# Optimization experiments

Measured on AMD Instinct MI355X. Metric: run time of the kernel, lower is better.

## Reference

```python
import jax, jax.numpy as jnp
import numpy as np

B, C, H, W = 16, 768, 32, 32
NH, HD, STRIDE = 12, 64, 2
ORF = 2.0  # offset_range_factor
EPS = 1e-5


def dwconv(x, w, b, s):
    # depthwise 3x3 conv, NCHW, weight [C,1,3,3]
    y = jax.lax.conv_general_dilated(
        x, w, window_strides=(s, s), padding=((1, 1), (1, 1)),
        dimension_numbers=('NCHW', 'OIHW', 'NCHW'), feature_group_count=x.shape[1])
    return y + b[None, :, None, None]


def layernorm_c(x, g, b):
    # LayerNorm over channel dim of NCHW (via bhwc as in LayerNormProxy)
    xt = jnp.transpose(x, (0, 2, 3, 1))
    mu = jnp.mean(xt, axis=-1, keepdims=True)
    var = jnp.mean((xt - mu) ** 2, axis=-1, keepdims=True)
    xn = (xt - mu) / jnp.sqrt(var + EPS)
    return jnp.transpose(xn * g + b, (0, 3, 1, 2))


def ref_points(Hh, Ww):
    # matches torch linspace(0.5, H-0.5, H)/H*2-1, stacked as (y, x)
    ry = (jnp.arange(Hh, dtype=jnp.float32) + 0.5) / Hh * 2.0 - 1.0
    rx = (jnp.arange(Ww, dtype=jnp.float32) + 0.5) / Ww * 2.0 - 1.0
    yy, xx = jnp.meshgrid(ry, rx, indexing='ij')
    return jnp.stack([yy, xx], axis=-1)  # [H, W, 2]


def grid_sample_bilinear(inp, grid):
    # inp [B,Cc,Hi,Wi], grid [B,Hg,Wg,2] in (x,y), align_corners=True, zeros padding
    Bb, Cc, Hi, Wi = inp.shape
    gx = (grid[..., 0] + 1.0) * (Wi - 1) * 0.5
    gy = (grid[..., 1] + 1.0) * (Hi - 1) * 0.5
    x0 = jnp.floor(gx); y0 = jnp.floor(gy)
    wx = gx - x0; wy = gy - y0

    def gather(iy, ix):
        valid = (ix >= 0) & (ix <= Wi - 1) & (iy >= 0) & (iy <= Hi - 1)
        iyc = jnp.clip(iy, 0, Hi - 1).astype(jnp.int32)
        ixc = jnp.clip(ix, 0, Wi - 1).astype(jnp.int32)
        vals = jax.vmap(lambda img, a, b: img[:, a, b])(inp, iyc, ixc)  # [B,Cc,Hg,Wg]
        return vals * valid[:, None, :, :].astype(inp.dtype)

    w00 = ((1 - wy) * (1 - wx))[:, None]
    w01 = ((1 - wy) * wx)[:, None]
    w10 = (wy * (1 - wx))[:, None]
    w11 = (wy * wx)[:, None]
    return (gather(y0, x0) * w00 + gather(y0, x0 + 1) * w01
            + gather(y0 + 1, x0) * w10 + gather(y0 + 1, x0 + 1) * w11)


def setup_inputs() -> dict:
    key = jax.random.key(0)
    ks = jax.random.split(key, 16)
    n = lambda k, shp, s: jax.random.normal(k, shp, jnp.float32) * s
    Hk = H // STRIDE
    return {
        'x': n(ks[0], (B, C, H, W), 1.0),
        'wv': n(ks[1], (C, 1, 3, 3), 0.1), 'bv': jnp.zeros((C,), jnp.float32),
        'wq': n(ks[2], (C, 1, 3, 3), 0.1), 'bq': jnp.zeros((C,), jnp.float32),
        'wk': n(ks[3], (C, 1, 3, 3), 0.1), 'bk': jnp.zeros((C,), jnp.float32),
        'w_off1': n(ks[4], (C, 1, 3, 3), 0.1), 'b_off1': jnp.zeros((C,), jnp.float32),
        'ln_g': jnp.ones((C,), jnp.float32), 'ln_b': jnp.zeros((C,), jnp.float32),
        'w_off2': n(ks[5], (2, C, 1, 1), 0.02),
        'rpe_table': n(ks[6], (NH, 2 * Hk - 1, 2 * Hk - 1), 0.01),
        'w_out': n(ks[7], (C, C, 1, 1), 0.02),
    }


def reference(x, wv, bv, wq, bq, wk, bk, w_off1, b_off1, ln_g, ln_b, w_off2, rpe_table, w_out):
    scale = HD ** -0.5
    value = dwconv(x, wv, bv, 1)          # [B,C,H,W]
    query = dwconv(x, wq, bq, 1)          # [B,C,H,W]
    keym = dwconv(x, wk, bk, STRIDE)      # [B,C,Hk,Wk]
    # offset branch: dwconv -> LN -> GELU -> 1x1 conv to 2 channels
    t = jax.nn.gelu(layernorm_c(dwconv(x, w_off1, b_off1, STRIDE), ln_g, ln_b), approximate=False)
    off = jnp.einsum('bchw,pc->bphw', t, w_off2.reshape(2, C))  # [B,2,Hk,Wk] (y,x)
    Hk, Wk = off.shape[2], off.shape[3]
    ns = Hk * Wk
    orange = jnp.array([1.0 / Hk, 1.0 / Wk], jnp.float32).reshape(1, 2, 1, 1)
    off = jnp.tanh(off) * orange * ORF
    off = jnp.transpose(off, (0, 2, 3, 1))  # [B,Hk,Wk,2]
    pos = off + ref_points(Hk, Wk)[None]    # [B,Hk,Wk,2] (y,x); ORF>0 -> no extra tanh

    vs = grid_sample_bilinear(value, pos[..., ::-1]).reshape(B * NH, HD, ns)
    q = query.reshape(B * NH, HD, H * W)
    k = keym.reshape(B * NH, HD, ns)
    attn = jnp.einsum('bcm,bcn->bmn', q, k) * scale  # [B*NH, HW, ns]

    # continuous relative position bias via grid_sample on rpe table
    rpe_bias = jnp.broadcast_to(rpe_table[None], (B, NH, 2 * Hk - 1, 2 * Wk - 1))
    qg = ref_points(H, W).reshape(H * W, 2)
    disp = (qg[None, :, None, :] - pos.reshape(B, ns, 2)[:, None, :, :]) * 0.5  # [B,HW,ns,2]
    bias = grid_sample_bilinear(rpe_bias, disp[..., ::-1]).reshape(B * NH, H * W, ns)

    attn = jax.nn.softmax(attn + bias, axis=-1)
    out = jnp.einsum('bmn,bcn->bcm', attn, vs).reshape(B, C, H, W)
    return jnp.einsum('bchw,oc->bohw', out, w_out.reshape(C, C))
```

## Files before the change

kernel.cpp:

```cpp
#include <hip/hip_runtime.h>
#include <hip/hip_bf16.h>
#include <math.h>

typedef unsigned short u16;
typedef __attribute__((ext_vector_type(8))) short bf8_t;
typedef __attribute__((ext_vector_type(4))) float f4_t;

#define BB 16
#define CC 768
#define HH 32
#define WW 32
#define HWL 1024
#define NHH 12
#define HDD 64
#define HK 16
#define NS 256
#define RT 31

__device__ inline float us2f(u16 u) {
    return __uint_as_float(((unsigned int)u) << 16);
}
__device__ inline u16 f2us(float f) {
    unsigned int u = __float_as_uint(f);
    unsigned int r = (u + 0x7fffu + ((u >> 16) & 1u)) >> 16;
    return (u16)r;
}

__global__ __launch_bounds__(256) void k_dwconv(
    const float* __restrict__ x,
    const float* __restrict__ wv, const float* __restrict__ bv,
    const float* __restrict__ wq, const float* __restrict__ bq,
    const float* __restrict__ wk, const float* __restrict__ bk,
    const float* __restrict__ wo, const float* __restrict__ bo,
    u16* __restrict__ value, u16* __restrict__ query,
    u16* __restrict__ key, float* __restrict__ tbuf)
{
    __shared__ float xs[34 * 34];
    int blk = blockIdx.x;
    int b = blk / CC, c = blk % CC;
    int tid = threadIdx.x;
    const float* xp = x + (size_t)(b * CC + c) * HWL;

    for (int i = tid; i < 34 * 34; i += 256) {
        int r = i / 34, cc2 = i % 34;
        int gr = r - 1, gc = cc2 - 1;
        float v = 0.f;
        if (gr >= 0 && gr < 32 && gc >= 0 && gc < 32) v = xp[gr * 32 + gc];
        xs[i] = v;
    }
    float wv_[9], wq_[9], wk_[9], wo_[9];
#pragma unroll
    for (int k = 0; k < 9; ++k) {
        wv_[k] = wv[c * 9 + k];
        wq_[k] = wq[c * 9 + k];
        wk_[k] = wk[c * 9 + k];
        wo_[k] = wo[c * 9 + k];
    }
    float bv_ = bv[c], bq_ = bq[c], bk_ = bk[c], bo_ = bo[c];
    __syncthreads();

    {
        int oy = tid >> 3;
        int ox4 = (tid & 7) * 4;
        float xw[3][6];
#pragma unroll
        for (int dy = 0; dy < 3; ++dy)
#pragma unroll
            for (int dx = 0; dx < 6; ++dx)
                xw[dy][dx] = xs[(oy + dy) * 34 + ox4 + dx];
        union { u16 u[4]; ushort4 v; } pv, pq;
#pragma unroll
        for (int j = 0; j < 4; ++j) {
            float av = 0.f, aq = 0.f;
#pragma unroll
            for (int dy = 0; dy < 3; ++dy)
#pragma unroll
                for (int dx = 0; dx < 3; ++dx) {
                    float xv = xw[dy][j + dx];
                    av += xv * wv_[dy * 3 + dx];
                    aq += xv * wq_[dy * 3 + dx];
                }
            pv.u[j] = f2us(av + bv_);
            pq.u[j] = f2us(aq + bq_);
        }
        size_t o = (size_t)(b * CC + c) * HWL + oy * 32 + ox4;
        *(ushort4*)&value[o] = pv.v;
        *(ushort4*)&query[o] = pq.v;
    }
    {
        int oy = tid >> 4, ox = tid & 15;
        float ak = 0.f, ao2 = 0.f;
#pragma unroll
        for (int dy = 0; dy < 3; ++dy)
#pragma unroll
            for (int dx = 0; dx < 3; ++dx) {
                float xv = xs[(2 * oy + dy) * 34 + 2 * ox + dx];
                ak += xv * wk_[dy * 3 + dx];
                ao2 += xv * wo_[dy * 3 + dx];
            }
        key[(size_t)(b * CC + c) * NS + tid] = f2us(ak + bk_);
        tbuf[(size_t)(b * CC + c) * NS + tid] = ao2 + bo_;
    }
}

__global__ __launch_bounds__(256) void k_offset(
    const float* __restrict__ tbuf,
    const float* __restrict__ lng, const float* __restrict__ lnb,
    const float* __restrict__ woff2, float* __restrict__ pos)
{
    __shared__ float sm[16];
    int blk = blockIdx.x;
    int b = blk >> 8;
    int n = blk & 255;
    int tid = threadIdx.x;
    const float* tp = tbuf + (size_t)b * CC * NS + n;
    float tv0 = tp[(size_t)tid * NS];
    float tv1 = tp[(size_t)(tid + 256) * NS];
    float tv2 = tp[(size_t)(tid + 512) * NS];
    float s = tv0 + tv1 + tv2;
    float sq = tv0 * tv0 + tv1 * tv1 + tv2 * tv2;
    for (int o = 32; o; o >>= 1) { s += __shfl_down(s, o); sq += __shfl_down(sq, o); }
    int w = tid >> 6;
    if ((tid & 63) == 0) { sm[w] = s; sm[4 + w] = sq; }
    __syncthreads();
    float st = sm[0] + sm[1] + sm[2] + sm[3];
    float sqt = sm[4] + sm[5] + sm[6] + sm[7];
    float mean = st * (1.f / 768.f);
    float var = sqt * (1.f / 768.f) - mean * mean;
    float rstd = rsqrtf(fmaxf(var, 0.f) + 1e-5f);

    float oy = 0.f, ox = 0.f;
#pragma unroll
    for (int j = 0; j < 3; ++j) {
        int c = tid + j * 256;
        float tvj = (j == 0) ? tv0 : ((j == 1) ? tv1 : tv2);
        float xn = (tvj - mean) * rstd;
        float y = xn * lng[c] + lnb[c];
        float ge = 0.5f * y * (1.f + erff(y * 0.70710678118654752f));
        oy += ge * woff2[c];
        ox += ge * woff2[CC + c];
    }
    for (int o = 32; o; o >>= 1) { oy += __shfl_down(oy, o); ox += __shfl_down(ox, o); }
    __syncthreads();
    if ((tid & 63) == 0) { sm[w] = oy; sm[8 + w] = ox; }
    __syncthreads();
    if (tid == 0) {
        float oyt = sm[0] + sm[1] + sm[2] + sm[3];
        float oxt = sm[8] + sm[9] + sm[10] + sm[11];
        float offy = tanhf(oyt) * 0.125f;
        float offx = tanhf(oxt) * 0.125f;
        int ky = n >> 4, kx = n & 15;
        pos[blk * 2 + 0] = (ky + 0.5f) * 0.125f - 1.f + offy;
        pos[blk * 2 + 1] = (kx + 0.5f) * 0.125f - 1.f + offx;
    }
}

__global__ __launch_bounds__(256) void k_sample(
    const u16* __restrict__ value, const float* __restrict__ pos,
    u16* __restrict__ vst)
{
    __shared__ float psl[NS * 2];
    int cg = blockIdx.x;
    int b  = blockIdx.y;
    int tid = threadIdx.x;
    for (int i = tid; i < NS * 2; i += 256) psl[i] = pos[b * NS * 2 + i];
    __syncthreads();
    int c = cg * 4 + (tid >> 6);
    int nl = tid & 63;
    const u16* vp = value + (size_t)(b * CC + c) * HWL;
    u16* op = vst + (size_t)(b * CC + c) * NS;
#pragma unroll
    for (int j = 0; j < 4; ++j) {
        int n = j * 64 + nl;
        float py = psl[2 * n], px = psl[2 * n + 1];
        float gx = (px + 1.f) * 15.5f;
        float gy = (py + 1.f) * 15.5f;
        float fx = floorf(gx), fy = floorf(gy);
        float wx = gx - fx, wy = gy - fy;
        int ix0 = (int)fx, iy0 = (int)fy;
        int ix1 = ix0 + 1, iy1 = iy0 + 1;
        float m00 = ((unsigned)ix0 < 32u && (unsigned)iy0 < 32u) ? 1.f : 0.f;
        float m01 = ((unsigned)ix1 < 32u && (unsigned)iy0 < 32u) ? 1.f : 0.f;
        float m10 = ((unsigned)ix0 < 32u && (unsigned)iy1 < 32u) ? 1.f : 0.f;
        float m11 = ((unsigned)ix1 < 32u && (unsigned)iy1 < 32u) ? 1.f : 0.f;
        int cx0 = min(max(ix0, 0), 31), cx1 = min(max(ix1, 0), 31);
        int cy0 = min(max(iy0, 0), 31), cy1 = min(max(iy1, 0), 31);
        float w00 = (1.f - wy) * (1.f - wx) * m00;
        float w01 = (1.f - wy) * wx * m01;
        float w10 = wy * (1.f - wx) * m10;
        float w11 = wy * wx * m11;
        float r = w00 * us2f(vp[cy0 * 32 + cx0]) + w01 * us2f(vp[cy0 * 32 + cx1])
                + w10 * us2f(vp[cy1 * 32 + cx0]) + w11 * us2f(vp[cy1 * 32 + cx1]);
        op[n] = f2us(r);
    }
}

__global__ __launch_bounds__(256) void k_transpose(
    const u16* __restrict__ in, u16* __restrict__ out, int R, int S)
{
    __shared__ u16 tile[64][68];
    int bx = blockIdx.x;
    int by = blockIdx.y;
    int bz = blockIdx.z;
    int t = threadIdx.x;
    int ci = (t & 15) * 4;
    int ri = t >> 4;
    const u16* ip = in + (size_t)bz * R * S;
    u16* op = out + (size_t)bz * R * S;
#pragma unroll
    for (int i = 0; i < 4; ++i) {
        int r = ri + i * 16;
        ushort4 v = *(const ushort4*)(ip + (size_t)(by * 64 + r) * S + bx * 64 + ci);
        *(ushort4*)&tile[r][ci] = v;
    }
    __syncthreads();
#pragma unroll
    for (int i = 0; i < 4; ++i) {
        int s = ri + i * 16;
        ushort4 v;
        v.x = tile[ci + 0][s];
        v.y = tile[ci + 1][s];
        v.z = tile[ci + 2][s];
        v.w = tile[ci + 3][s];
        *(ushort4*)(op + (size_t)(bx * 64 + s) * R + by * 64 + ci) = v;
    }
}

__global__ __launch_bounds__(256) void k_cvtw(
    const float* __restrict__ w, u16* __restrict__ wbf)
{
    int i = (blockIdx.x * 256 + threadIdx.x) * 4;
    float4 v = *(const float4*)(w + i);
    union { u16 u[4]; ushort4 v; } pk;
    pk.u[0] = f2us(v.x); pk.u[1] = f2us(v.y);
    pk.u[2] = f2us(v.z); pk.u[3] = f2us(v.w);
    *(ushort4*)(wbf + i) = pk.v;
}

__global__ __launch_bounds__(256, 4) void k_attn(
    const u16* __restrict__ query, const u16* __restrict__ kt,
    const u16* __restrict__ vst, const float* __restrict__ rpe,
    const float* __restrict__ pos, u16* __restrict__ ao)
{
    __shared__ float2 tabp2[35 * 36];
    __shared__ float2 psl2[NS];
    __shared__ u16 Plds[4][16][72];

    int L = blockIdx.x;
    int xcd = L & 7;
    int t2 = L >> 3;
    int mt = t2 & 15;
    int bh = xcd + 8 * (t2 >> 4);
    int b = bh / NHH, h = bh % NHH;
    int tid = threadIdx.x;
    int w = tid >> 6;
    int l = tid & 63;
    int li = l & 15, lg4 = l >> 4;

    for (int i = tid; i < 35 * 36; i += 256) {
        int r = i / 36, c = i % 36;
        int rr = r - 2;
        int c0i = c - 2, c1i = c - 1;
        float v0 = ((unsigned)rr < 31u && (unsigned)c0i < 31u)
                       ? rpe[h * RT * RT + rr * RT + c0i] : 0.f;
        float v1 = ((unsigned)rr < 31u && (unsigned)c1i < 31u)
                       ? rpe[h * RT * RT + rr * RT + c1i] : 0.f;
        tabp2[i] = make_float2(v0, v1);
    }
    for (int i = tid; i < NS; i += 256) {
        psl2[i] = make_float2(pos[b * NS * 2 + 2 * i], pos[b * NS * 2 + 2 * i + 1]);
    }
    __syncthreads();

    int m0 = mt * 64 + w * 16;
    int c0 = h * 64;

    bf8_t qf[2];
#pragma unroll
    for (int ks = 0; ks < 2; ++ks) {
        union { short s[8]; bf8_t v; } u;
#pragma unroll
        for (int j = 0; j < 8; ++j)
            u.s[j] = (short)query[(size_t)(b * CC + c0 + ks * 32 + lg4 * 8 + j) * HWL + m0 + li];
        qf[ks] = u.v;
    }
    bf8_t ones;
    {
        union { short s[8]; bf8_t v; } u;
#pragma unroll
        for (int j = 0; j < 8; ++j) u.s[j] = (short)0x3F80;
        ones = u.v;
    }

    f4_t O[4];
#pragma unroll
    for (int ci = 0; ci < 4; ++ci) O[ci] = (f4_t){0.f, 0.f, 0.f, 0.f};
    float mrun[4], lrun[4];
#pragma unroll
    for (int r = 0; r < 4; ++r) { mrun[r] = -1e30f; lrun[r] = 0.f; }

    int mrow = m0 + lg4 * 4;
    float qgy  = ((mrow >> 5) + 0.5f) * 0.0625f - 1.f;
    float qgx0 = ((mrow & 31) + 0.5f) * 0.0625f - 1.f;

    for (int chunk = 0; chunk < 4; ++chunk) {
        int n0 = chunk * 64;
        bf8_t kf[4][2];
#pragma unroll
        for (int ni = 0; ni < 4; ++ni)
#pragma unroll
            for (int ks = 0; ks < 2; ++ks)
                kf[ni][ks] = *(const bf8_t*)(kt + (size_t)(b * NS + n0 + ni * 16 + li) * CC + c0 + ks * 32 + lg4 * 8);

        f4_t s[4];
#pragma unroll
        for (int ni = 0; ni < 4; ++ni) {
            f4_t acc = (f4_t){0.f, 0.f, 0.f, 0.f};
            acc = __builtin_amdgcn_mfma_f32_16x16x32_bf16(qf[0], kf[ni][0], acc, 0, 0, 0);
            acc = __builtin_amdgcn_mfma_f32_16x16x32_bf16(qf[1], kf[ni][1], acc, 0, 0, 0);
            s[ni] = acc;
        }

#pragma unroll
        for (int ni = 0; ni < 4; ++ni) {
            int n = n0 + ni * 16 + li;
            float2 p2 = psl2[n];
            float gy = ((qgy - p2.x) * 0.5f + 1.f) * 15.f;
            float fy = floorf(gy);
            float wy = gy - fy;
            int iy = (int)fy;
            float gxb = (qgx0 - p2.y) * 7.5f + 15.f;
            const float2* row0 = &tabp2[(iy + 2) * 36 + 2];
#pragma unroll
            for (int r = 0; r < 4; ++r) {
                float gx = gxb + r * 0.46875f;
                float fx = floorf(gx);
                float wx = gx - fx;
                int ix = (int)fx;
                float2 t0 = row0[ix];
                float2 t1 = row0[ix + 36];
                float bias = (1.f - wy) * ((1.f - wx) * t0.x + wx * t0.y)
                           + wy * ((1.f - wx) * t1.x + wx * t1.y);
                s[ni][r] = s[ni][r] * 0.125f + bias;
            }
        }

#pragma unroll
        for (int r = 0; r < 4; ++r) {
            float v = fmaxf(fmaxf(s[0][r], s[1][r]), fmaxf(s[2][r], s[3][r]));
            v = fmaxf(v, __shfl_xor(v, 1));
            v = fmaxf(v, __shfl_xor(v, 2));
            v = fmaxf(v, __shfl_xor(v, 4));
            v = fmaxf(v, __shfl_xor(v, 8));
            float mnew = fmaxf(mrun[r], v);
            float sc = __expf(mrun[r] - mnew);
            mrun[r] = mnew;
            lrun[r] *= sc;
#pragma unroll
            for (int ni = 0; ni < 4; ++ni)
                s[ni][r] = __expf(s[ni][r] - mnew);
#pragma unroll
            for (int ci = 0; ci < 4; ++ci) O[ci][r] *= sc;
        }
#pragma unroll
        for (int ni = 0; ni < 4; ++ni)
#pragma unroll
            for (int r = 0; r < 4; ++r)
                Plds[w][lg4 * 4 + r][ni * 16 + li] = f2us(s[ni][r]);

        bf8_t pf[2];
#pragma unroll
        for (int ks = 0; ks < 2; ++ks)
            pf[ks] = *(const bf8_t*)&Plds[w][li][ks * 32 + lg4 * 8];

        f4_t ps = (f4_t){0.f, 0.f, 0.f, 0.f};
        ps = __builtin_amdgcn_mfma_f32_16x16x32_bf16(pf[0], ones, ps, 0, 0, 0);
        ps = __builtin_amdgcn_mfma_f32_16x16x32_bf16(pf[1], ones, ps, 0, 0, 0);
#pragma unroll
        for (int r = 0; r < 4; ++r) lrun[r] += ps[r];

        bf8_t vf[4][2];
#pragma unroll
        for (int ci = 0; ci < 4; ++ci)
#pragma unroll
            for (int ks = 0; ks < 2; ++ks)
                vf[ci][ks] = *(const bf8_t*)(vst + (size_t)(b * CC + c0 + ci * 16 + li) * NS + n0 + ks * 32 + lg4 * 8);
#pragma unroll
        for (int ci = 0; ci < 4; ++ci) {
            O[ci] = __builtin_amdgcn_mfma_f32_16x16x32_bf16(pf[0], vf[ci][0], O[ci], 0, 0, 0);
            O[ci] = __builtin_amdgcn_mfma_f32_16x16x32_bf16(pf[1], vf[ci][1], O[ci], 0, 0, 0);
        }
    }
    float inv[4];
#pragma unroll
    for (int r = 0; r < 4; ++r) inv[r] = 1.f / lrun[r];
#pragma unroll
    for (int ci = 0; ci < 4; ++ci)
#pragma unroll
        for (int r = 0; r < 4; ++r) {
            int m = m0 + lg4 * 4 + r;
            ao[(size_t)(b * HWL + m) * CC + c0 + ci * 16 + li] = f2us(O[ci][r] * inv[r]);
        }
}

__global__ __launch_bounds__(256) void k_proj(
    const u16* __restrict__ ao, const u16* __restrict__ wbf,
    float* __restrict__ out)
{
    int L = blockIdx.x;
    int xcd = L & 7;
    int t = L >> 3;
    int ot = t % 6;
    int gh = t / 6;
    int g = xcd + 8 * gh;
    int mt = g & 7;
    int b = g >> 3;
    int tid = threadIdx.x;
    int w = tid >> 6, l = tid & 63;
    int li = l & 15, lg4 = l >> 4;
    int o0 = ot * 128 + (w >> 1) * 64;
    int m0 = mt * 128 + (w & 1) * 64;

    const u16* ap = ao + (size_t)b * HWL * CC;

    f4_t acc[4][4];
#pragma unroll
    for (int i = 0; i < 4; ++i)
#pragma unroll
        for (int j = 0; j < 4; ++j) acc[i][j] = (f4_t){0.f, 0.f, 0.f, 0.f};

#pragma unroll 2
    for (int kc = 0; kc < CC; kc += 64) {
        bf8_t af[4][2], bfr[4][2];
#pragma unroll
        for (int i = 0; i < 4; ++i)
#pragma unroll
            for (int ks = 0; ks < 2; ++ks) {
                af[i][ks]  = *(const bf8_t*)(wbf + (size_t)(o0 + i * 16 + li) * CC + kc + ks * 32 + lg4 * 8);
                bfr[i][ks] = *(const bf8_t*)(ap  + (size_t)(m0 + i * 16 + li) * CC + kc + ks * 32 + lg4 * 8);
            }
#pragma unroll
        for (int i = 0; i < 4; ++i)
#pragma unroll
            for (int j = 0; j < 4; ++j) {
                acc[i][j] = __builtin_amdgcn_mfma_f32_16x16x32_bf16(af[i][0], bfr[j][0], acc[i][j], 0, 0, 0);
                acc[i][j] = __builtin_amdgcn_mfma_f32_16x16x32_bf16(af[i][1], bfr[j][1], acc[i][j], 0, 0, 0);
            }
    }
#pragma unroll
    for (int i = 0; i < 4; ++i)
#pragma unroll
        for (int r = 0; r < 4; ++r) {
            int o = o0 + i * 16 + lg4 * 4 + r;
            float* op = out + ((size_t)b * CC + o) * HWL + m0;
#pragma unroll
            for (int j = 0; j < 4; ++j)
                op[j * 16 + li] = acc[i][j][r];
        }
}

extern "C" void kernel_launch(void* const* d_in, const int* in_sizes, int n_in,
                              void* d_out, int out_size, void* d_ws, size_t ws_size,
                              hipStream_t stream) {
    const float* x     = (const float*)d_in[0];
    const float* wv    = (const float*)d_in[1];
    const float* bv    = (const float*)d_in[2];
    const float* wq    = (const float*)d_in[3];
    const float* bq    = (const float*)d_in[4];
    const float* wk    = (const float*)d_in[5];
    const float* bk    = (const float*)d_in[6];
    const float* wo1   = (const float*)d_in[7];
    const float* bo1   = (const float*)d_in[8];
    const float* lng   = (const float*)d_in[9];
    const float* lnb   = (const float*)d_in[10];
    const float* woff2 = (const float*)d_in[11];
    const float* rpe   = (const float*)d_in[12];
    const float* wout  = (const float*)d_in[13];
    float* out = (float*)d_out;

    char* ws = (char*)d_ws;
    size_t off = 0;
    auto alloc = [&](size_t nbytes) -> void* {
        void* p = ws + off;
        off += (nbytes + 255) & ~(size_t)255;
        return p;
    };
    u16*   value = (u16*)  alloc((size_t)BB * CC * HWL * 2);
    u16*   query = (u16*)  alloc((size_t)BB * CC * HWL * 2);
    u16*   key   = (u16*)  alloc((size_t)BB * CC * NS * 2);
    float* tbuf  = (float*)alloc((size_t)BB * NS * CC * 4);
    float* pos   = (float*)alloc((size_t)BB * NS * 2 * 4);
    u16*   ao    = (u16*)  alloc((size_t)BB * HWL * CC * 2);
    u16*   wbf   = (u16*)  alloc((size_t)CC * CC * 2);

    u16* kt  = (u16*)tbuf;
    u16* vst = (u16*)((char*)tbuf + (size_t)BB * NS * CC * 2);

    k_dwconv<<<BB * CC, 256, 0, stream>>>(x, wv, bv, wq, bq, wk, bk, wo1, bo1,
                                          value, query, key, tbuf);
    k_offset<<<BB * NS, 256, 0, stream>>>(tbuf, lng, lnb, woff2, pos);
    k_sample<<<dim3(CC / 4, BB), 256, 0, stream>>>(value, pos, vst);
    k_transpose<<<dim3(NS / 64, CC / 64, BB), 256, 0, stream>>>(key, kt, CC, NS);
    k_cvtw<<<CC * CC / 1024, 256, 0, stream>>>(wout, wbf);
    k_attn<<<dim3(16 * 192), 256, 0, stream>>>(query, kt, vst, rpe, pos, ao);
    k_proj<<<dim3(768), 256, 0, stream>>>(ao, wbf, out);
}
```

Before: 235.0 us.

## Stage K/V tiles in swizzled LDS with register prefetch of next chunk

Each block now cooperatively loads the 64x64 K and V tiles for the current chunk into XOR-swizzled shared memory, and every wave reads its MFMA fragments from there instead of issuing its own global loads. The next chunk's tiles are prefetched into registers while the current chunk computes, then written to LDS between barriers. This removes the four-fold redundant global traffic across the block's waves and hides load latency. In exchange it adds 16KB of LDS per block, which may lower occupancy, plus two barriers per chunk.

```diff
diff --git a/kernel.cpp b/kernel.cpp
--- a/kernel.cpp
+++ b/kernel.cpp
@@ -4,6 +4,7 @@
 
 typedef unsigned short u16;
 typedef __attribute__((ext_vector_type(8))) short bf8_t;
+typedef __attribute__((ext_vector_type(8))) unsigned short us8_t;
 typedef __attribute__((ext_vector_type(4))) float f4_t;
 
 #define BB 16
@@ -245,6 +246,8 @@
     __shared__ float2 tabp2[35 * 36];
     __shared__ float2 psl2[NS];
     __shared__ u16 Plds[4][16][72];
+    __shared__ u16 KsS[4096];
+    __shared__ u16 VsS[4096];
 
     int L = blockIdx.x;
     int xcd = L & 7;
@@ -270,10 +273,23 @@
     for (int i = tid; i < NS; i += 256) {
         psl2[i] = make_float2(pos[b * NS * 2 + 2 * i], pos[b * NS * 2 + 2 * i + 1]);
     }
+
+    int c0 = h * 64;
+
+#pragma unroll
+    for (int it = 0; it < 2; ++it) {
+        int Li = tid + it * 256;
+        int row = Li >> 3;
+        int colb = (Li & 7) * 16;
+        us8_t kv = *(const us8_t*)(kt  + (size_t)(b * NS + row) * CC + c0 + colb / 2);
+        us8_t vv = *(const us8_t*)(vst + (size_t)(b * CC + c0 + row) * NS + colb / 2);
+        int so = (Li * 16) ^ ((row & 7) << 4);
+        *(us8_t*)((char*)KsS + so) = kv;
+        *(us8_t*)((char*)VsS + so) = vv;
+    }
     __syncthreads();
 
     int m0 = mt * 64 + w * 16;
-    int c0 = h * 64;
 
     bf8_t qf[2];
 #pragma unroll
@@ -305,12 +321,28 @@
 
     for (int chunk = 0; chunk < 4; ++chunk) {
         int n0 = chunk * 64;
+
         bf8_t kf[4][2];
 #pragma unroll
         for (int ni = 0; ni < 4; ++ni)
 #pragma unroll
-            for (int ks = 0; ks < 2; ++ks)
-                kf[ni][ks] = *(const bf8_t*)(kt + (size_t)(b * NS + n0 + ni * 16 + li) * CC + c0 + ks * 32 + lg4 * 8);
+            for (int ks = 0; ks < 2; ++ks) {
+                int addr = (ni * 16 + li) * 128 + ks * 64 + lg4 * 16;
+                kf[ni][ks] = *(const bf8_t*)((const char*)KsS + (addr ^ ((li & 7) << 4)));
+            }
+
+        us8_t nk[2], nv[2];
+        if (chunk < 3) {
+            int n1 = n0 + 64;
+#pragma unroll
+            for (int it = 0; it < 2; ++it) {
+                int Li = tid + it * 256;
+                int row = Li >> 3;
+                int colb = (Li & 7) * 16;
+                nk[it] = *(const us8_t*)(kt  + (size_t)(b * NS + n1 + row) * CC + c0 + colb / 2);
+                nv[it] = *(const us8_t*)(vst + (size_t)(b * CC + c0 + row) * NS + n1 + colb / 2);
+            }
+        }
 
         f4_t s[4];
 #pragma unroll
@@ -383,12 +415,27 @@
 #pragma unroll
         for (int ci = 0; ci < 4; ++ci)
 #pragma unroll
-            for (int ks = 0; ks < 2; ++ks)
-                vf[ci][ks] = *(const bf8_t*)(vst + (size_t)(b * CC + c0 + ci * 16 + li) * NS + n0 + ks * 32 + lg4 * 8);
+            for (int ks = 0; ks < 2; ++ks) {
+                int addr = (ci * 16 + li) * 128 + ks * 64 + lg4 * 16;
+                vf[ci][ks] = *(const bf8_t*)((const char*)VsS + (addr ^ ((li & 7) << 4)));
+            }
 #pragma unroll
         for (int ci = 0; ci < 4; ++ci) {
             O[ci] = __builtin_amdgcn_mfma_f32_16x16x32_bf16(pf[0], vf[ci][0], O[ci], 0, 0, 0);
             O[ci] = __builtin_amdgcn_mfma_f32_16x16x32_bf16(pf[1], vf[ci][1], O[ci], 0, 0, 0);
+        }
+
+        if (chunk < 3) {
+            __syncthreads();
+#pragma unroll
+            for (int it = 0; it < 2; ++it) {
+                int Li = tid + it * 256;
+                int row = Li >> 3;
+                int so = (Li * 16) ^ ((row & 7) << 4);
+                *(us8_t*)((char*)KsS + so) = nk[it];
+                *(us8_t*)((char*)VsS + so) = nv[it];
+            }
+            __syncthreads();
         }
     }
     float inv[4];
```

After: 194.4 us (median of 2 runs). 1.21x faster.
